# Performance work log

Measured on AMD Instinct MI355X. Metric: run time of the kernel, lower is better.

The kernel has to match this reference:

```python
import jax, jax.numpy as jnp
import numpy as np

FORMULA_OH_SIZES = [20, 20, 20, 20, 20]
SPECT_BIN_N = 512


def layer_norm(x, g, b, eps=1e-5):
    m = jnp.mean(x, axis=-1, keepdims=True)
    v = jnp.var(x, axis=-1, keepdims=True)
    return (x - m) * jax.lax.rsqrt(v + eps) * g + b


def gru_cell(x, h, W_ih, W_hh, b_ih, b_hh):
    # torch.nn.GRUCell math
    gi = x @ W_ih.T + b_ih
    gh = h @ W_hh.T + b_hh
    i_r, i_z, i_n = jnp.split(gi, 3, axis=-1)
    h_r, h_z, h_n = jnp.split(gh, 3, axis=-1)
    r = jax.nn.sigmoid(i_r + h_r)
    z = jax.nn.sigmoid(i_z + h_z)
    n = jnp.tanh(i_n + r * h_n)
    return (1.0 - z) * n + z * h


def structured_one_hot(x, sizes, accum=True):
    # x: [N, len(sizes)] integer element counts -> concatenated (accumulated) one-hots
    outs = []
    for i, s in enumerate(sizes):
        v = jnp.clip(x[:, i].astype(jnp.int32), 0, s - 1)
        if accum:
            oh = (jnp.arange(s)[None, :] <= v[:, None]).astype(jnp.float32)  # thermometer
        else:
            oh = jax.nn.one_hot(v, s, dtype=jnp.float32)
        outs.append(oh)
    return jnp.concatenate(outs, axis=-1)


def setup_inputs():
    key = jax.random.key(0)
    ks = jax.random.split(key, 16)
    B, A, GF, HW, S, M = 16, 32, 128, 4, 4096, 8
    G = GF * HW                       # 512 = g_feat_in * highway_steps_n
    FE = sum(FORMULA_OH_SIZES)        # 100
    D = 512                           # internal_d
    vert_feat_in = jax.random.normal(ks[0], (B, A, GF, HW), jnp.float32)
    vert_mask_in = jnp.ones((B, A), jnp.float32)
    elem_id = jax.random.randint(ks[1], (B, A), 0, 5)
    vert_element_oh = jax.nn.one_hot(elem_id, 5, dtype=jnp.float32)
    adj_oh = jnp.zeros((B, A, A, 4), jnp.float32)  # unused by forward
    atom_subsets = jax.random.bernoulli(ks[2], 0.5, (B, S, A)).astype(jnp.float32)
    masses = jax.random.uniform(ks[3], (B, S, M), jnp.float32, 0.0, SPECT_BIN_N - 1.0)
    intens = jax.random.uniform(ks[4], (B, S, M), jnp.float32)
    atom_subsets_peaks = jnp.stack([masses, intens], axis=-1)

    def lin(k, o, i):
        return (jax.random.normal(k, (o, i), jnp.float32) / np.sqrt(i)).astype(jnp.float32)

    return dict(
        vert_feat_in=vert_feat_in, vert_mask_in=vert_mask_in,
        vert_element_oh=vert_element_oh, adj_oh=adj_oh,
        atom_subsets=atom_subsets, atom_subsets_peaks=atom_subsets_peaks,
        ln_sub_g=jnp.ones((G,), jnp.float32), ln_sub_b=jnp.zeros((G,), jnp.float32),
        W_ih=lin(ks[5], 3 * G, FE), W_hh=lin(ks[6], 3 * G, G),
        b_ih=jnp.zeros((3 * G,), jnp.float32), b_hh=jnp.zeros((3 * G,), jnp.float32),
        W1=lin(ks[7], D, G), b1=jnp.zeros((D,), jnp.float32),
        W2a=lin(ks[8], D, D), b2a=jnp.zeros((D,), jnp.float32),
        W2b=lin(ks[9], D, D), b2b=jnp.zeros((D,), jnp.float32),
        ln_pre_g=jnp.ones((D,), jnp.float32), ln_pre_b=jnp.zeros((D,), jnp.float32),
        Ws=lin(ks[10], 1, D), bs=jnp.zeros((1,), jnp.float32),
    )


def reference(vert_feat_in, vert_mask_in, vert_element_oh, adj_oh, atom_subsets,
              atom_subsets_peaks, ln_sub_g, ln_sub_b, W_ih, W_hh, b_ih, b_hh,
              W1, b1, W2a, b2a, W2b, b2b, ln_pre_g, ln_pre_b, Ws, bs):
    B, A, GF, HW = vert_feat_in.shape
    S = atom_subsets.shape[1]
    vf = vert_feat_in.reshape(B, A, GF * HW)                       # [B,A,G]
    masked_vf = vf * vert_mask_in[:, :, None]
    subs_m = atom_subsets * vert_mask_in[:, None, :]               # [B,S,A]
    swvs = jnp.einsum('bag,bsa->bsg', masked_vf, subs_m)           # [B,S,G]
    # per-subset element counts -> structured one-hot formula encoding
    counts = jnp.einsum('bae,bsa->bse', vert_element_oh, atom_subsets).astype(jnp.int32)
    pf_flat = structured_one_hot(counts.reshape(B * S, -1), FORMULA_OH_SIZES, accum=True)
    subset_size = jnp.sum(subs_m, axis=2) + 1e-4                   # [B,S]
    mean = swvs / subset_size[:, :, None]
    normed = layer_norm(mean, ln_sub_g, ln_sub_b)                  # [B,S,G]
    h = gru_cell(pf_flat, normed.reshape(B * S, -1), W_ih, W_hh, b_ih, b_hh)
    h = h.reshape(normed.shape)
    x = jax.nn.relu(h @ W1.T + b1)
    x = jax.nn.relu(x @ W2a.T + b2a)
    x = jax.nn.relu(x @ W2b.T + b2b)   # (extra F.relu in original is idempotent)
    x = layer_norm(x, ln_pre_g, ln_pre_b)
    scores = (x @ Ws.T + bs)[..., 0]                               # [B,S]
    probs = jax.nn.softmax(scores, axis=-1)
    # mass histogram: scatter intensity*prob into rounded-mass bins
    masses = atom_subsets_peaks[..., 0]                            # [B,S,M]
    intens = atom_subsets_peaks[..., 1]
    bins = jnp.clip(jnp.round(masses).astype(jnp.int32), 0, SPECT_BIN_N - 1)
    contrib = intens * probs[:, :, None]                           # [B,S,M]
    spect = jnp.zeros((B, SPECT_BIN_N), x.dtype).at[
        jnp.arange(B)[:, None], bins.reshape(B, -1)].add(contrib.reshape(B, -1))
    return (spect, probs)
```

## Files before the change

### kernel.cpp

```cpp
#include <hip/hip_runtime.h>
#include <math.h>

#define B_ 16
#define A_ 32
#define G_ 512
#define S_ 4096
#define M_ 8
#define BS_ 65536
#define KC_ 640
#define NG_ 1536
#define SMH 16384

typedef _Float16 half8 __attribute__((ext_vector_type(8)));
typedef _Float16 half4v __attribute__((ext_vector_type(4)));
typedef _Float16 half2v __attribute__((ext_vector_type(2)));
typedef float floatx4 __attribute__((ext_vector_type(4)));

typedef const __attribute__((address_space(1))) void* gas_t;
typedef __attribute__((address_space(3))) void* las_t;

__device__ __forceinline__ float wave_sum_f(float v){
#pragma unroll
  for (int o = 32; o > 0; o >>= 1) v += __shfl_xor(v, o);
  return v;
}
__device__ __forceinline__ float wave_max_f(float v){
#pragma unroll
  for (int o = 32; o > 0; o >>= 1) v = fmaxf(v, __shfl_xor(v, o));
  return v;
}
__device__ __forceinline__ float sigmoidf_(float x){ return 1.f/(1.f+__expf(-x)); }
__device__ __forceinline__ float tanhf_(float x){ return 1.f - 2.f/(__expf(2.f*x)+1.f); }

__global__ __launch_bounds__(256) void k_cvt3(const float* __restrict__ s0,
                                              const float* __restrict__ s1,
                                              const float* __restrict__ s2,
                                              _Float16* __restrict__ d){
  const float* s = (blockIdx.y == 0) ? s0 : (blockIdx.y == 1) ? s1 : s2;
  int i = (blockIdx.x*256 + threadIdx.x)*4;
  if (i >= G_*G_) return;
  float4 v = *(const float4*)(s+i);
  half4v o; o[0]=(_Float16)v.x; o[1]=(_Float16)v.y; o[2]=(_Float16)v.z; o[3]=(_Float16)v.w;
  *(half4v*)(d + (size_t)blockIdx.y*G_*G_ + i) = o;
}

__global__ __launch_bounds__(64) void k_buildw(const float* __restrict__ Whh,
                                               const float* __restrict__ Wih,
                                               _Float16* __restrict__ Wcat){
  int j = blockIdx.x;
  for (int p = threadIdx.x; p < KC_; p += 64){
    float v = 0.f;
    if (p < 512) v = Whh[(size_t)j*512 + p];
    else if (p < 612) v = Wih[(size_t)j*100 + (p - 512)];
    Wcat[(size_t)j*KC_ + p] = (_Float16)v;
  }
}

__global__ __launch_bounds__(256) void k_prep_mfma(
    const float* __restrict__ vf, const float* __restrict__ mask,
    const float* __restrict__ eoh, const float* __restrict__ subs,
    const float* __restrict__ ln_g, const float* __restrict__ ln_b,
    _Float16* __restrict__ Abuf){
  __shared__ _Float16 s_mvfT[G_*A_];
  __shared__ _Float16 s_sm[128*A_];
  __shared__ float s_m[A_];
  __shared__ float s_e[A_*5];
  __shared__ float s_ssum[128];
  __shared__ float s_red1[2][4][16];
  __shared__ float s_red2[2][4][16];
  int tid = threadIdx.x;
  int bx = blockIdx.x, b = blockIdx.y;
  int lane = tid & 63, w = tid >> 6;
  int q = lane >> 4, l15 = lane & 15;
  size_t row0 = (size_t)b*S_ + (size_t)bx*128;
  if (tid < A_)   s_m[tid] = mask[b*A_ + tid];
  if (tid < A_*5) s_e[tid] = eoh[b*A_*5 + tid];
  __syncthreads();
  {
    int p = tid & 15, gseg = tid >> 4;
    float mk0 = s_m[2*p], mk1 = s_m[2*p+1];
    const float* v0 = vf + ((size_t)b*A_ + 2*p)*G_ + gseg*32;
    const float* v1 = v0 + G_;
#pragma unroll
    for (int i = 0; i < 32; i += 4){
      float4 a = *(const float4*)(v0 + i);
      float4 c = *(const float4*)(v1 + i);
      float av[4] = {a.x, a.y, a.z, a.w};
      float cv[4] = {c.x, c.y, c.z, c.w};
#pragma unroll
      for (int j = 0; j < 4; ++j){
        half2v h; h[0] = (_Float16)(av[j]*mk0); h[1] = (_Float16)(cv[j]*mk1);
        *(half2v*)(s_mvfT + (gseg*32 + i + j)*A_ + 2*p) = h;
      }
    }
  }
  {
    int s = tid >> 1, hh = tid & 1;
    const float* sp = subs + (row0 + s)*A_ + hh*16;
    _Float16* dst = s_sm + s*A_ + hh*16;
#pragma unroll
    for (int i = 0; i < 16; i += 4){
      float4 v = *(const float4*)(sp + i);
      half4v h; h[0]=(_Float16)v.x; h[1]=(_Float16)v.y; h[2]=(_Float16)v.z; h[3]=(_Float16)v.w;
      *(half4v*)(dst + i) = h;
    }
  }
  __syncthreads();
  if (tid < 128){
    int s = tid;
    float ssum = 0.f, c0=0.f, c1=0.f, c2=0.f, c3=0.f, c4=0.f;
#pragma unroll
    for (int a = 0; a < A_; ++a){
      float v = (float)s_sm[s*A_ + a];
      ssum += v * s_m[a];
      c0 += v * s_e[a*5+0]; c1 += v * s_e[a*5+1]; c2 += v * s_e[a*5+2];
      c3 += v * s_e[a*5+3]; c4 += v * s_e[a*5+4];
    }
    int cc[5];
    cc[0] = min(max((int)(c0+0.5f),0),19); cc[1] = min(max((int)(c1+0.5f),0),19);
    cc[2] = min(max((int)(c2+0.5f),0),19); cc[3] = min(max((int)(c3+0.5f),0),19);
    cc[4] = min(max((int)(c4+0.5f),0),19);
    s_ssum[s] = ssum;
    _Float16* dst = Abuf + (row0 + s)*KC_ + 512;
#pragma unroll
    for (int t = 0; t < 16; ++t){
      half8 hv;
#pragma unroll
      for (int u = 0; u < 8; ++u){
        int k = t*8 + u;
        float v = 0.f;
        if (k < 100){ int f = k/20, l = k - f*20; v = (l <= cc[f]) ? 1.f : 0.f; }
        hv[u] = (_Float16)v;
      }
      *(half8*)(dst + t*8) = hv;
    }
  }
  half8 bf[8]; float lng[8], lnb[8];
#pragma unroll
  for (int t = 0; t < 8; ++t){
    int g = w*128 + t*16 + l15;
    bf[t] = *(const half8*)(s_mvfT + g*A_ + q*8);
    lng[t] = ln_g[g]; lnb[t] = ln_b[g];
  }
  __syncthreads();
  for (int gi = 0; gi < 8; ++gi){
    half8 af = *(const half8*)(s_sm + (gi*16 + l15)*A_ + q*8);
    floatx4 c[8];
#pragma unroll
    for (int t = 0; t < 8; ++t){
      floatx4 z = {0.f, 0.f, 0.f, 0.f};
      c[t] = __builtin_amdgcn_mfma_f32_16x16x32_f16(af, bf[t], z, 0, 0, 0);
    }
    float p1[4] = {0.f,0.f,0.f,0.f}, p2[4] = {0.f,0.f,0.f,0.f};
#pragma unroll
    for (int t = 0; t < 8; ++t)
#pragma unroll
      for (int r = 0; r < 4; ++r){ float v = c[t][r]; p1[r] += v; p2[r] += v*v; }
#pragma unroll
    for (int off = 1; off < 16; off <<= 1)
#pragma unroll
      for (int r = 0; r < 4; ++r){
        p1[r] += __shfl_xor(p1[r], off);
        p2[r] += __shfl_xor(p2[r], off);
      }
    int gb = gi & 1;
    if (l15 == 0){
#pragma unroll
      for (int r = 0; r < 4; ++r){ s_red1[gb][w][q*4+r] = p1[r]; s_red2[gb][w][q*4+r] = p2[r]; }
    }
    __syncthreads();
#pragma unroll
    for (int r = 0; r < 4; ++r){
      int sl = gi*16 + q*4 + r;
      int rr = q*4 + r;
      float t1 = s_red1[gb][0][rr] + s_red1[gb][1][rr] + s_red1[gb][2][rr] + s_red1[gb][3][rr];
      float t2 = s_red2[gb][0][rr] + s_red2[gb][1][rr] + s_red2[gb][2][rr] + s_red2[gb][3][rr];
      float inv = 1.f/(s_ssum[sl] + 1e-4f);
      float mu = t1*inv*(1.f/512.f);
      float var = t2*inv*inv*(1.f/512.f) - mu*mu;
      float rs = rsqrtf(var + 1e-5f);
      _Float16* orow = Abuf + (row0 + sl)*KC_;
#pragma unroll
      for (int t = 0; t < 8; ++t){
        float o = (c[t][r]*inv - mu)*rs*lng[t] + lnb[t];
        orow[w*128 + t*16 + l15] = (_Float16)o;
      }
    }
  }
}

__global__ __launch_bounds__(512) void k_gru_fused(
    const _Float16* __restrict__ Abuf, const _Float16* __restrict__ Wcat,
    const float* __restrict__ bih, const float* __restrict__ bhh,
    _Float16* __restrict__ H){
  __shared__ _Float16 smA[2][128*32];
  __shared__ _Float16 smB[2][192*32];
  int tid = threadIdx.x;
  int lane = tid & 63, wvid = tid >> 6;
  int wm = wvid & 1, wn = wvid >> 1;
  int q = lane >> 4, l15 = lane & 15;
  int mt = blockIdx.x*64 + (blockIdx.y >> 3);
  int dt = blockIdx.y & 7;
  int m0 = mt*128, n0 = dt*64;
  floatx4 acc[3][4] = {};
  floatx4 accNI[4] = {};
  int offA[4], offB[3];
#pragma unroll
  for (int i = 0; i < 4; ++i){
    int r = wm*64 + i*16 + l15;
    offA[i] = (r*4 + (q ^ ((r>>2)&3)))*8;
  }
#pragma unroll
  for (int g = 0; g < 3; ++g){
    int rb = g*64 + wn*16 + l15;
    offB[g] = (rb*4 + (q ^ ((rb>>2)&3)))*8;
  }
  const _Float16* gA;
  {
    int u = wvid*64 + lane;
    int r = u >> 2, c = (u & 3) ^ ((r >> 2) & 3);
    gA = Abuf + (size_t)(m0 + r)*KC_ + c*8;
  }
  const _Float16* gB0;
  {
    int u = wvid*64 + lane;
    int rb = u >> 2, c = (u & 3) ^ ((rb >> 2) & 3);
    int grow = (rb >> 6)*512 + n0 + (rb & 63);
    gB0 = Wcat + (size_t)grow*KC_ + c*8;
  }
  const _Float16* gB1 = nullptr;
  if (wvid < 4){
    int u = (8 + wvid)*64 + lane;
    int rb = u >> 2, c = (u & 3) ^ ((rb >> 2) & 3);
    int grow = (rb >> 6)*512 + n0 + (rb & 63);
    gB1 = Wcat + (size_t)grow*KC_ + c*8;
  }
  __builtin_amdgcn_global_load_lds((gas_t)gA,  (las_t)(smA[0] + wvid*512), 16, 0, 0);
  __builtin_amdgcn_global_load_lds((gas_t)gB0, (las_t)(smB[0] + wvid*512), 16, 0, 0);
  if (wvid < 4)
    __builtin_amdgcn_global_load_lds((gas_t)gB1, (las_t)(smB[0] + (8+wvid)*512), 16, 0, 0);
  asm volatile("s_waitcnt vmcnt(0)");
  __builtin_amdgcn_s_barrier();
  const int NT = KC_/32;
  for (int t = 0; t < NT; ++t){
    int cur = t & 1;
    if (t + 1 < NT){
      int kc = (t+1)*32;
      __builtin_amdgcn_global_load_lds((gas_t)(gA + kc),  (las_t)(smA[cur^1] + wvid*512), 16, 0, 0);
      __builtin_amdgcn_global_load_lds((gas_t)(gB0 + kc), (las_t)(smB[cur^1] + wvid*512), 16, 0, 0);
      if (wvid < 4)
        __builtin_amdgcn_global_load_lds((gas_t)(gB1 + kc), (las_t)(smB[cur^1] + (8+wvid)*512), 16, 0, 0);
    }
    half8 af[4], bfv[3];
#pragma unroll
    for (int i = 0; i < 4; ++i) af[i] = *(const half8*)(smA[cur] + offA[i]);
#pragma unroll
    for (int g = 0; g < 3; ++g) bfv[g] = *(const half8*)(smB[cur] + offB[g]);
    if (t < 16){
#pragma unroll
      for (int g = 0; g < 3; ++g)
#pragma unroll
        for (int i = 0; i < 4; ++i)
          acc[g][i] = __builtin_amdgcn_mfma_f32_16x16x32_f16(af[i], bfv[g], acc[g][i], 0, 0, 0);
    } else {
#pragma unroll
      for (int i = 0; i < 4; ++i){
        acc[0][i] = __builtin_amdgcn_mfma_f32_16x16x32_f16(af[i], bfv[0], acc[0][i], 0, 0, 0);
        acc[1][i] = __builtin_amdgcn_mfma_f32_16x16x32_f16(af[i], bfv[1], acc[1][i], 0, 0, 0);
        accNI[i]  = __builtin_amdgcn_mfma_f32_16x16x32_f16(af[i], bfv[2], accNI[i], 0, 0, 0);
      }
    }
    asm volatile("s_waitcnt vmcnt(0)");
    __builtin_amdgcn_s_barrier();
  }
  int d = n0 + wn*16 + l15;
  float br  = bih[d] + bhh[d];
  float bz  = bih[512+d] + bhh[512+d];
  float bnh = bhh[1024+d];
  float bni = bih[1024+d];
#pragma unroll
  for (int i = 0; i < 4; ++i){
#pragma unroll
    for (int r = 0; r < 4; ++r){
      int m = m0 + wm*64 + i*16 + q*4 + r;
      float gr  = acc[0][i][r] + br;
      float gz  = acc[1][i][r] + bz;
      float hn  = acc[2][i][r] + bnh;
      float in_ = accNI[i][r] + bni;
      float rrv = sigmoidf_(gr);
      float zz  = sigmoidf_(gz);
      float nn  = tanhf_(in_ + rrv*hn);
      float hp  = (float)Abuf[(size_t)m*KC_ + d];
      H[(size_t)m*G_ + d] = (_Float16)((1.f-zz)*nn + zz*hp);
    }
  }
}


#define STG_A8(T) do{ \
    __builtin_amdgcn_global_load_lds((gas_t)(pA0 + (T)*64),           (las_t)(&smA8[(T)&1][0] + wvid*1024),        16, 0, 0); \
    __builtin_amdgcn_global_load_lds((gas_t)(pA1 + (T)*64),           (las_t)(&smA8[(T)&1][0] + wvid*1024 + 512),  16, 0, 0); \
    __builtin_amdgcn_global_load_lds((gas_t)(pA0 + 128*G_ + (T)*64),  (las_t)(&smA8[(T)&1][0] + 8192 + wvid*1024), 16, 0, 0); \
    __builtin_amdgcn_global_load_lds((gas_t)(pA1 + 128*G_ + (T)*64),  (las_t)(&smA8[(T)&1][0] + 8192 + wvid*1024 + 512), 16, 0, 0); \
  }while(0)
#define STG_B8(T,H) do{ \
    __builtin_amdgcn_global_load_lds((gas_t)(pB0 + (H)*128*G_ + (T)*64), (las_t)(&smB8[(T)&1][0] + (H)*8192 + wvid*1024),       16, 0, 0); \
    __builtin_amdgcn_global_load_lds((gas_t)(pB1 + (H)*128*G_ + (T)*64), (las_t)(&smB8[(T)&1][0] + (H)*8192 + wvid*1024 + 512), 16, 0, 0); \
  }while(0)
#define RD_A8(DST, T, MF0) do{ \
    const _Float16* ba_ = &smA8[(T)&1][0]; \
    DST[0][0] = *(const half8*)(ba_ + aoff0 + (MF0)*1024); \
    DST[0][1] = *(const half8*)(ba_ + aoff1 + (MF0)*1024); \
    DST[1][0] = *(const half8*)(ba_ + aoff0 + ((MF0)+1)*1024); \
    DST[1][1] = *(const half8*)(ba_ + aoff1 + ((MF0)+1)*1024); \
  }while(0)
#define RD_B8(DST, T) do{ \
    const _Float16* bb_ = &smB8[(T)&1][0]; \
    _Pragma("unroll") \
    for (int nf_ = 0; nf_ < 4; ++nf_){ \
      DST[nf_][0] = *(const half8*)(bb_ + boff0 + nf_*1024); \
      DST[nf_][1] = *(const half8*)(bb_ + boff1 + nf_*1024); \
    } \
  }while(0)
#define MMQ8(AV, BV, MF0) do{ \
    _Pragma("unroll") \
    for (int u_ = 0; u_ < 2; ++u_) \
    _Pragma("unroll") \
    for (int nf_ = 0; nf_ < 4; ++nf_){ \
      acc[(MF0)+u_][nf_] = __builtin_amdgcn_mfma_f32_16x16x32_f16(AV[u_][0], BV[nf_][0], acc[(MF0)+u_][nf_], 0, 0, 0); \
      acc[(MF0)+u_][nf_] = __builtin_amdgcn_mfma_f32_16x16x32_f16(AV[u_][1], BV[nf_][1], acc[(MF0)+u_][nf_], 0, 0, 0); \
    } \
  }while(0)
#define PH_Q0(T, BC) do{ if ((T)+1 <= 7) STG_A8((T)+1); RD_A8(a_o, T, 2); \
    __builtin_amdgcn_s_barrier(); __builtin_amdgcn_s_setprio(1); MMQ8(a_e, BC, 0); \
    __builtin_amdgcn_s_setprio(0); __builtin_amdgcn_s_barrier(); }while(0)
#define PH_Q1(T, BC) do{ if ((T)+2 <= 7) STG_B8((T)+2, 0); RD_A8(a_e, T, 4); \
    __builtin_amdgcn_s_barrier(); __builtin_amdgcn_s_setprio(1); MMQ8(a_o, BC, 2); \
    __builtin_amdgcn_s_setprio(0); __builtin_amdgcn_s_barrier(); }while(0)
#define PH_Q2(T, BC) do{ if ((T)+2 <= 7) STG_B8((T)+2, 1); RD_A8(a_o, T, 6); \
    __builtin_amdgcn_s_barrier(); __builtin_amdgcn_s_setprio(1); MMQ8(a_e, BC, 4); \
    __builtin_amdgcn_s_setprio(0); __builtin_amdgcn_s_barrier(); }while(0)
#define PH_Q3(T, BC, BN) do{ \
    if ((T) < 7){ \
      if ((T) < 6) asm volatile("s_waitcnt vmcnt(4)" ::: "memory"); \
      else         asm volatile("s_waitcnt vmcnt(0)" ::: "memory"); \
      RD_B8(BN, (T)+1); RD_A8(a_e, (T)+1, 0); \
    } \
    __builtin_amdgcn_s_barrier(); __builtin_amdgcn_s_setprio(1); MMQ8(a_o, BC, 6); \
    __builtin_amdgcn_s_setprio(0); __builtin_amdgcn_s_barrier(); }while(0)
#define TILE8(T, BC, BN) do{ PH_Q0(T, BC); PH_Q1(T, BC); PH_Q2(T, BC); PH_Q3(T, BC, BN); }while(0)

#define K8_SETUP(Amat, Wmat) \
  int tid = threadIdx.x; \
  int lane = tid & 63, wvid = tid >> 6; \
  int wm = wvid & 1, wn = wvid >> 1; \
  int q = lane >> 4, l15 = lane & 15; \
  int x_ = l15 & 7; \
  int bid = blockIdx.x; \
  int wg = (bid & 7)*64 + (bid >> 3); \
  int mt = wg >> 1, nt = wg & 1; \
  int m0 = mt*256, n0 = nt*256; \
  int swzlo = (q ^ (x_ & 3))*8; \
  int aoff0 = (wm*128 + l15)*64 + ((0 ^ (x_>>2))*4)*8 + swzlo; \
  int aoff1 = (wm*128 + l15)*64 + ((1 ^ (x_>>2))*4)*8 + swzlo; \
  int boff0 = (wn*64 + l15)*64 + ((0 ^ (x_>>2))*4)*8 + swzlo; \
  int boff1 = (wn*64 + l15)*64 + ((1 ^ (x_>>2))*4)*8 + swzlo; \
  int srow = wvid*16 + (lane >> 3); \
  int sc = ((lane & 7) ^ ((lane >> 3) & 7))*8; \
  const _Float16* pA0 = Amat + (size_t)(m0 + srow)*G_ + sc; \
  const _Float16* pA1 = Amat + (size_t)(m0 + srow + 8)*G_ + sc; \
  const _Float16* pB0 = Wmat + (size_t)(n0 + srow)*G_ + sc; \
  const _Float16* pB1 = Wmat + (size_t)(n0 + srow + 8)*G_ + sc; \
  floatx4 acc[8][4] = {}; \
  half8 a_e[2][2], a_o[2][2], bA[4][2], bB[4][2]; \
  STG_A8(0); STG_B8(0,0); STG_B8(0,1); STG_B8(1,0); STG_B8(1,1); \
  asm volatile("s_waitcnt vmcnt(4)" ::: "memory"); \
  __builtin_amdgcn_s_barrier(); \
  RD_B8(bA, 0); RD_A8(a_e, 0, 0); \
  TILE8(0, bA, bB); TILE8(1, bB, bA); \
  TILE8(2, bA, bB); TILE8(3, bB, bA); \
  TILE8(4, bA, bB); TILE8(5, bB, bA); \
  TILE8(6, bA, bB); TILE8(7, bB, bA);

__global__ __launch_bounds__(512, 2) void k_gemm8(
    const _Float16* __restrict__ A, const _Float16* __restrict__ W,
    const float* __restrict__ bias, _Float16* __restrict__ Out){
  __shared__ _Float16 smA8[2][SMH];
  __shared__ _Float16 smB8[2][SMH];
  K8_SETUP(A, W)
  float bv[4];
#pragma unroll
  for (int nf = 0; nf < 4; ++nf) bv[nf] = bias[n0 + wn*64 + nf*16 + l15];
#pragma unroll
  for (int mf = 0; mf < 8; ++mf){
    int m = m0 + wm*128 + mf*16 + q*4;
#pragma unroll
    for (int nf = 0; nf < 4; ++nf){
      int n = n0 + wn*64 + nf*16 + l15;
#pragma unroll
      for (int r = 0; r < 4; ++r)
        Out[(size_t)(m+r)*G_ + n] = (_Float16)fmaxf(acc[mf][nf][r] + bv[nf], 0.f);
    }
  }
}

__global__ __launch_bounds__(512, 2) void k_ff38(
    const _Float16* __restrict__ A, const _Float16* __restrict__ W,
    const float* __restrict__ bias, const float* __restrict__ ln_pre_g,
    const float* __restrict__ Ws, float* __restrict__ Pbuf){
  __shared__ _Float16 smA8[2][SMH];
  __shared__ _Float16 smB8[2][SMH];
  K8_SETUP(A, W)
  float gws[4], bv[4];
#pragma unroll
  for (int nf = 0; nf < 4; ++nf){
    int n = n0 + wn*64 + nf*16 + l15;
    gws[nf] = ln_pre_g[n]*Ws[n];
    bv[nf] = bias[n];
  }
  float* sP = (float*)&smB8[0][0];
#pragma unroll
  for (int mf = 0; mf < 8; ++mf){
#pragma unroll
    for (int r = 0; r < 4; ++r){
      float p1 = 0.f, p2 = 0.f, p3 = 0.f;
#pragma unroll
      for (int nf = 0; nf < 4; ++nf){
        float xv = fmaxf(acc[mf][nf][r] + bv[nf], 0.f);
        p1 += xv; p2 += xv*xv; p3 += gws[nf]*xv;
      }
#pragma unroll
      for (int off = 1; off < 16; off <<= 1){
        p1 += __shfl_xor(p1, off);
        p2 += __shfl_xor(p2, off);
        p3 += __shfl_xor(p3, off);
      }
      if (l15 == 0){
        int rl = wm*128 + mf*16 + q*4 + r;
        sP[(rl*4 + wn)*3 + 0] = p1;
        sP[(rl*4 + wn)*3 + 1] = p2;
        sP[(rl*4 + wn)*3 + 2] = p3;
      }
    }
  }
  __syncthreads();
  if (tid < 256){
    int m = m0 + tid;
    float* dst = Pbuf + ((size_t)m*2 + nt)*3;
#pragma unroll
    for (int c = 0; c < 3; ++c)
      dst[c] = sP[(tid*4+0)*3+c] + sP[(tid*4+1)*3+c] +
               sP[(tid*4+2)*3+c] + sP[(tid*4+3)*3+c];
  }
}

__global__ __launch_bounds__(256) void k_score_fin(
    const float* __restrict__ Pbuf, const float* __restrict__ g,
    const float* __restrict__ bta, const float* __restrict__ Ws,
    const float* __restrict__ bs, float* __restrict__ scores,
    float* __restrict__ spect){
  __shared__ float red[8];
  int tid = threadIdx.x, lane = tid & 63, wv = tid >> 6;
  if (blockIdx.x < 32) spect[(size_t)blockIdx.x*256 + tid] = 0.f;
  int i0 = tid*2;
  float c1p = g[i0]*Ws[i0] + g[i0+1]*Ws[i0+1];
  float c2p = bta[i0]*Ws[i0] + bta[i0+1]*Ws[i0+1];
  c1p = wave_sum_f(c1p); c2p = wave_sum_f(c2p);
  if (lane == 0){ red[wv] = c1p; red[4+wv] = c2p; }
  __syncthreads();
  float c1 = red[0]+red[1]+red[2]+red[3];
  float c2 = red[4]+red[5]+red[6]+red[7] + bs[0];
  size_t row = (size_t)blockIdx.x*256 + tid;
  const float* p = Pbuf + row*6;
  float2 u0 = *(const float2*)p;
  float2 u1 = *(const float2*)(p+2);
  float2 u2 = *(const float2*)(p+4);
  float P1 = u0.x + u1.y;
  float P2 = u0.y + u2.x;
  float P3 = u1.x + u2.y;
  float mu = P1*(1.f/512.f);
  float var = P2*(1.f/512.f) - mu*mu;
  float rs = rsqrtf(var + 1e-5f);
  scores[row] = rs*(P3 - mu*c1) + c2;
}

__global__ __launch_bounds__(256) void k_softmax(
    const float* __restrict__ scores, float* __restrict__ probs){
  __shared__ float red[4];
  int b = blockIdx.x, tid = threadIdx.x, lane = tid & 63, wv = tid >> 6;
  const float* sp = scores + (size_t)b*S_;
  float* pp = probs + (size_t)b*S_;
  float mx = -1e30f;
  for (int i = tid; i < S_; i += 256) mx = fmaxf(mx, sp[i]);
  mx = wave_max_f(mx);
  if (lane == 0) red[wv] = mx;
  __syncthreads();
  mx = fmaxf(fmaxf(red[0], red[1]), fmaxf(red[2], red[3]));
  __syncthreads();
  float sum = 0.f;
  for (int i = tid; i < S_; i += 256){
    float e = __expf(sp[i]-mx);
    pp[i] = e;
    sum += e;
  }
  sum = wave_sum_f(sum);
  if (lane == 0) red[wv] = sum;
  __syncthreads();
  sum = red[0]+red[1]+red[2]+red[3];
  float inv = 1.f/sum;
  for (int i = tid; i < S_; i += 256)
    pp[i] *= inv;
}

__global__ __launch_bounds__(256) void k_spect_p(
    const float* __restrict__ peaks, const float* __restrict__ probs,
    float* __restrict__ spect){
  __shared__ float bins[512];
  int b = blockIdx.x, chunk = blockIdx.y, tid = threadIdx.x;
  bins[tid] = 0.f; bins[tid+256] = 0.f;
  __syncthreads();
  int s0 = chunk*(S_/8);
  for (int i = tid; i < (S_/8)*M_; i += 256){
    int s = s0 + (i >> 3), m = i & 7;
    const float* pk = peaks + (((size_t)b*S_ + s)*M_ + m)*2;
    float mass = pk[0], inten = pk[1];
    float p = probs[(size_t)b*S_ + s];
    int bin = (int)rintf(mass);
    bin = min(max(bin, 0), 511);
    atomicAdd(&bins[bin], inten*p);
  }
  __syncthreads();
  atomicAdd(&spect[(size_t)b*512 + tid],       bins[tid]);
  atomicAdd(&spect[(size_t)b*512 + tid + 256], bins[tid+256]);
}

extern "C" void kernel_launch(void* const* d_in, const int* in_sizes, int n_in,
                              void* d_out, int out_size, void* d_ws, size_t ws_size,
                              hipStream_t stream) {
  const float* vf       = (const float*)d_in[0];
  const float* mask     = (const float*)d_in[1];
  const float* eoh      = (const float*)d_in[2];
  const float* subs     = (const float*)d_in[4];
  const float* peaks    = (const float*)d_in[5];
  const float* ln_sub_g = (const float*)d_in[6];
  const float* ln_sub_b = (const float*)d_in[7];
  const float* W_ih     = (const float*)d_in[8];
  const float* W_hh     = (const float*)d_in[9];
  const float* b_ih     = (const float*)d_in[10];
  const float* b_hh     = (const float*)d_in[11];
  const float* W1       = (const float*)d_in[12];
  const float* b1       = (const float*)d_in[13];
  const float* W2a      = (const float*)d_in[14];
  const float* b2a      = (const float*)d_in[15];
  const float* W2b      = (const float*)d_in[16];
  const float* b2b      = (const float*)d_in[17];
  const float* ln_pre_g = (const float*)d_in[18];
  const float* ln_pre_b = (const float*)d_in[19];
  const float* Ws       = (const float*)d_in[20];
  const float* bs       = (const float*)d_in[21];
  float* out = (float*)d_out;
  float* probs_out = out + (size_t)B_*512;

  char* w = (char*)d_ws;
  float* scores = (float*)w;     w += (size_t)BS_*4;
  float* Pbuf   = (float*)w;     w += (size_t)BS_*12*4;
  _Float16* Wcat = (_Float16*)w; w += (size_t)NG_*KC_*2;
  _Float16* W1h  = (_Float16*)w; w += (size_t)G_*G_*2;
  _Float16* W2ah = (_Float16*)w; w += (size_t)G_*G_*2;
  _Float16* W2bh = (_Float16*)w; w += (size_t)G_*G_*2;
  _Float16* Abuf = (_Float16*)w; w += (size_t)BS_*KC_*2;
  _Float16* bufh0 = (_Float16*)w;
  _Float16* bufh1 = Abuf;

  k_cvt3<<<dim3((G_*G_/4+255)/256, 3), 256, 0, stream>>>(W1, W2a, W2b, W1h);
  k_buildw<<<NG_, 64, 0, stream>>>(W_hh, W_ih, Wcat);
  k_prep_mfma<<<dim3(S_/128, B_), 256, 0, stream>>>(vf, mask, eoh, subs,
                                                    ln_sub_g, ln_sub_b, Abuf);
  k_gru_fused<<<dim3(8, 512), 512, 0, stream>>>(Abuf, Wcat, b_ih, b_hh, bufh0);
  k_gemm8<<<512, 512, 0, stream>>>(bufh0, W1h,  b1,  bufh1);
  k_gemm8<<<512, 512, 0, stream>>>(bufh1, W2ah, b2a, bufh0);
  k_ff38<<<512, 512, 0, stream>>>(bufh0, W2bh, b2b, ln_pre_g, Ws, Pbuf);
  k_score_fin<<<BS_/256, 256, 0, stream>>>(Pbuf, ln_pre_g, ln_pre_b, Ws, bs,
                                           scores, out);
  k_softmax<<<B_, 256, 0, stream>>>(scores, probs_out);
  k_spect_p<<<dim3(B_, 8), 256, 0, stream>>>(peaks, probs_out, out);
}
```

Before: 470.0 us.

## Rewrite GRU GEMM with 256-row tiles, 64-wide K stages, and phased software pipeline

```diff
diff --git a/kernel.cpp b/kernel.cpp
--- a/kernel.cpp
+++ b/kernel.cpp
@@ -189,104 +189,120 @@
   }
 }
 
-__global__ __launch_bounds__(512) void k_gru_fused(
+#define GSTG_A(T) do{ \
+    __builtin_amdgcn_global_load_lds((gas_t)(qA0 + (T)*64),            (las_t)(&gmA[(T)&1][0] + wvid*1024),        16, 0, 0); \
+    __builtin_amdgcn_global_load_lds((gas_t)(qA1 + (T)*64),            (las_t)(&gmA[(T)&1][0] + wvid*1024 + 512),  16, 0, 0); \
+    __builtin_amdgcn_global_load_lds((gas_t)(qA0 + 128*KC_ + (T)*64),  (las_t)(&gmA[(T)&1][0] + 8192 + wvid*1024), 16, 0, 0); \
+    __builtin_amdgcn_global_load_lds((gas_t)(qA1 + 128*KC_ + (T)*64),  (las_t)(&gmA[(T)&1][0] + 8192 + wvid*1024 + 512), 16, 0, 0); \
+  }while(0)
+#define GSTG_B(T) do{ \
+    __builtin_amdgcn_global_load_lds((gas_t)(qB0 + (T)*64), (las_t)(&gmB[(T)&1][0] + wvid*1536),        16, 0, 0); \
+    __builtin_amdgcn_global_load_lds((gas_t)(qB1 + (T)*64), (las_t)(&gmB[(T)&1][0] + wvid*1536 + 512),  16, 0, 0); \
+    __builtin_amdgcn_global_load_lds((gas_t)(qB2 + (T)*64), (las_t)(&gmB[(T)&1][0] + wvid*1536 + 1024), 16, 0, 0); \
+  }while(0)
+#define GRD_A(DST, T, MF0) do{ \
+    const _Float16* ba_ = &gmA[(T)&1][0]; \
+    DST[0][0] = *(const half8*)(ba_ + aoff0 + (MF0)*1024); \
+    DST[0][1] = *(const half8*)(ba_ + aoff1 + (MF0)*1024); \
+    DST[1][0] = *(const half8*)(ba_ + aoff0 + ((MF0)+1)*1024); \
+    DST[1][1] = *(const half8*)(ba_ + aoff1 + ((MF0)+1)*1024); \
+  }while(0)
+#define GRD_B(DST, T) do{ \
+    const _Float16* bb_ = &gmB[(T)&1][0]; \
+    _Pragma("unroll") \
+    for (int g_ = 0; g_ < 3; ++g_){ \
+      DST[g_][0] = *(const half8*)(bb_ + bo0[g_]); \
+      DST[g_][1] = *(const half8*)(bb_ + bo1[g_]); \
+    } \
+  }while(0)
+#define GMMQ(AV, BV, MF0, G2) do{ \
+    _Pragma("unroll") \
+    for (int u_ = 0; u_ < 2; ++u_){ \
+      acc[(MF0)+u_][0]  = __builtin_amdgcn_mfma_f32_16x16x32_f16(AV[u_][0], BV[0][0], acc[(MF0)+u_][0], 0, 0, 0); \
+      acc[(MF0)+u_][0]  = __builtin_amdgcn_mfma_f32_16x16x32_f16(AV[u_][1], BV[0][1], acc[(MF0)+u_][0], 0, 0, 0); \
+      acc[(MF0)+u_][1]  = __builtin_amdgcn_mfma_f32_16x16x32_f16(AV[u_][0], BV[1][0], acc[(MF0)+u_][1], 0, 0, 0); \
+      acc[(MF0)+u_][1]  = __builtin_amdgcn_mfma_f32_16x16x32_f16(AV[u_][1], BV[1][1], acc[(MF0)+u_][1], 0, 0, 0); \
+      acc[(MF0)+u_][G2] = __builtin_amdgcn_mfma_f32_16x16x32_f16(AV[u_][0], BV[2][0], acc[(MF0)+u_][G2], 0, 0, 0); \
+      acc[(MF0)+u_][G2] = __builtin_amdgcn_mfma_f32_16x16x32_f16(AV[u_][1], BV[2][1], acc[(MF0)+u_][G2], 0, 0, 0); \
+    } \
+  }while(0)
+#define GPH0(T, BC, G2) do{ if ((T)+1 <= 9) GSTG_A((T)+1); GRD_A(a_o, T, 2); \
+    __builtin_amdgcn_s_barrier(); __builtin_amdgcn_s_setprio(1); GMMQ(a_e, BC, 0, G2); \
+    __builtin_amdgcn_s_setprio(0); __builtin_amdgcn_s_barrier(); }while(0)
+#define GPH1(T, BC, G2) do{ if ((T)+2 <= 9) GSTG_B((T)+2); GRD_A(a_e, T, 4); \
+    __builtin_amdgcn_s_barrier(); __builtin_amdgcn_s_setprio(1); GMMQ(a_o, BC, 2, G2); \
+    __builtin_amdgcn_s_setprio(0); __builtin_amdgcn_s_barrier(); }while(0)
+#define GPH2(T, BC, G2) do{ GRD_A(a_o, T, 6); \
+    __builtin_amdgcn_s_barrier(); __builtin_amdgcn_s_setprio(1); GMMQ(a_e, BC, 4, G2); \
+    __builtin_amdgcn_s_setprio(0); __builtin_amdgcn_s_barrier(); }while(0)
+#define GPH3(T, BC, BN, G2) do{ \
+    if ((T) < 9){ \
+      if ((T)+2 <= 9) asm volatile("s_waitcnt vmcnt(3)" ::: "memory"); \
+      else            asm volatile("s_waitcnt vmcnt(0)" ::: "memory"); \
+      GRD_B(BN, (T)+1); GRD_A(a_e, (T)+1, 0); \
+    } \
+    __builtin_amdgcn_s_barrier(); __builtin_amdgcn_s_setprio(1); GMMQ(a_o, BC, 6, G2); \
+    __builtin_amdgcn_s_setprio(0); __builtin_amdgcn_s_barrier(); }while(0)
+#define GTILE(T, BC, BN, G2) do{ GPH0(T, BC, G2); GPH1(T, BC, G2); GPH2(T, BC, G2); GPH3(T, BC, BN, G2); }while(0)
+
+__global__ __launch_bounds__(512, 2) void k_gru8(
     const _Float16* __restrict__ Abuf, const _Float16* __restrict__ Wcat,
     const float* __restrict__ bih, const float* __restrict__ bhh,
     _Float16* __restrict__ H){
-  __shared__ _Float16 smA[2][128*32];
-  __shared__ _Float16 smB[2][192*32];
+  __shared__ _Float16 gmA[2][SMH];
+  __shared__ _Float16 gmB[2][192*64];
   int tid = threadIdx.x;
   int lane = tid & 63, wvid = tid >> 6;
   int wm = wvid & 1, wn = wvid >> 1;
   int q = lane >> 4, l15 = lane & 15;
-  int mt = blockIdx.x*64 + (blockIdx.y >> 3);
-  int dt = blockIdx.y & 7;
-  int m0 = mt*128, n0 = dt*64;
-  floatx4 acc[3][4] = {};
-  floatx4 accNI[4] = {};
-  int offA[4], offB[3];
-#pragma unroll
-  for (int i = 0; i < 4; ++i){
-    int r = wm*64 + i*16 + l15;
-    offA[i] = (r*4 + (q ^ ((r>>2)&3)))*8;
-  }
+  int x_ = l15 & 7;
+  int bid = blockIdx.x;
+  int mt = (bid & 7)*32 + (bid >> 6);
+  int dt = (bid >> 3) & 7;
+  int m0 = mt*256, d0 = dt*64;
+  int swzlo = (q ^ (x_ & 3))*8;
+  int aoff0 = (wm*128 + l15)*64 + ((0 ^ (x_>>2))*4)*8 + swzlo;
+  int aoff1 = (wm*128 + l15)*64 + ((1 ^ (x_>>2))*4)*8 + swzlo;
+  int bo0[3], bo1[3];
 #pragma unroll
   for (int g = 0; g < 3; ++g){
-    int rb = g*64 + wn*16 + l15;
-    offB[g] = (rb*4 + (q ^ ((rb>>2)&3)))*8;
-  }
-  const _Float16* gA;
-  {
-    int u = wvid*64 + lane;
-    int r = u >> 2, c = (u & 3) ^ ((r >> 2) & 3);
-    gA = Abuf + (size_t)(m0 + r)*KC_ + c*8;
-  }
-  const _Float16* gB0;
-  {
-    int u = wvid*64 + lane;
-    int rb = u >> 2, c = (u & 3) ^ ((rb >> 2) & 3);
-    int grow = (rb >> 6)*512 + n0 + (rb & 63);
-    gB0 = Wcat + (size_t)grow*KC_ + c*8;
-  }
-  const _Float16* gB1 = nullptr;
-  if (wvid < 4){
-    int u = (8 + wvid)*64 + lane;
-    int rb = u >> 2, c = (u & 3) ^ ((rb >> 2) & 3);
-    int grow = (rb >> 6)*512 + n0 + (rb & 63);
-    gB1 = Wcat + (size_t)grow*KC_ + c*8;
-  }
-  __builtin_amdgcn_global_load_lds((gas_t)gA,  (las_t)(smA[0] + wvid*512), 16, 0, 0);
-  __builtin_amdgcn_global_load_lds((gas_t)gB0, (las_t)(smB[0] + wvid*512), 16, 0, 0);
-  if (wvid < 4)
-    __builtin_amdgcn_global_load_lds((gas_t)gB1, (las_t)(smB[0] + (8+wvid)*512), 16, 0, 0);
-  asm volatile("s_waitcnt vmcnt(0)");
+    int rb = (g*64 + wn*16 + l15)*64;
+    bo0[g] = rb + ((0 ^ (x_>>2))*4)*8 + swzlo;
+    bo1[g] = rb + ((1 ^ (x_>>2))*4)*8 + swzlo;
+  }
+  int srow = wvid*16 + (lane >> 3);
+  int sc = ((lane & 7) ^ ((lane >> 3) & 7))*8;
+  const _Float16* qA0 = Abuf + (size_t)(m0 + srow)*KC_ + sc;
+  const _Float16* qA1 = Abuf + (size_t)(m0 + srow + 8)*KC_ + sc;
+  int rb0 = wvid*24 + (lane >> 3);
+  const _Float16* qB0 = Wcat + (size_t)(((rb0    )>>6)*512 + d0 + ((rb0    )&63))*KC_ + sc;
+  const _Float16* qB1 = Wcat + (size_t)(((rb0+ 8)>>6)*512 + d0 + ((rb0+ 8)&63))*KC_ + sc;
+  const _Float16* qB2 = Wcat + (size_t)(((rb0+16)>>6)*512 + d0 + ((rb0+16)&63))*KC_ + sc;
+  floatx4 acc[8][4] = {};
+  half8 a_e[2][2], a_o[2][2], bA[3][2], bB[3][2];
+  GSTG_A(0); GSTG_B(0); GSTG_B(1);
+  asm volatile("s_waitcnt vmcnt(3)" ::: "memory");
   __builtin_amdgcn_s_barrier();
-  const int NT = KC_/32;
-  for (int t = 0; t < NT; ++t){
-    int cur = t & 1;
-    if (t + 1 < NT){
-      int kc = (t+1)*32;
-      __builtin_amdgcn_global_load_lds((gas_t)(gA + kc),  (las_t)(smA[cur^1] + wvid*512), 16, 0, 0);
-      __builtin_amdgcn_global_load_lds((gas_t)(gB0 + kc), (las_t)(smB[cur^1] + wvid*512), 16, 0, 0);
-      if (wvid < 4)
-        __builtin_amdgcn_global_load_lds((gas_t)(gB1 + kc), (las_t)(smB[cur^1] + (8+wvid)*512), 16, 0, 0);
-    }
-    half8 af[4], bfv[3];
-#pragma unroll
-    for (int i = 0; i < 4; ++i) af[i] = *(const half8*)(smA[cur] + offA[i]);
-#pragma unroll
-    for (int g = 0; g < 3; ++g) bfv[g] = *(const half8*)(smB[cur] + offB[g]);
-    if (t < 16){
-#pragma unroll
-      for (int g = 0; g < 3; ++g)
-#pragma unroll
-        for (int i = 0; i < 4; ++i)
-          acc[g][i] = __builtin_amdgcn_mfma_f32_16x16x32_f16(af[i], bfv[g], acc[g][i], 0, 0, 0);
-    } else {
-#pragma unroll
-      for (int i = 0; i < 4; ++i){
-        acc[0][i] = __builtin_amdgcn_mfma_f32_16x16x32_f16(af[i], bfv[0], acc[0][i], 0, 0, 0);
-        acc[1][i] = __builtin_amdgcn_mfma_f32_16x16x32_f16(af[i], bfv[1], acc[1][i], 0, 0, 0);
-        accNI[i]  = __builtin_amdgcn_mfma_f32_16x16x32_f16(af[i], bfv[2], accNI[i], 0, 0, 0);
-      }
-    }
-    asm volatile("s_waitcnt vmcnt(0)");
-    __builtin_amdgcn_s_barrier();
-  }
-  int d = n0 + wn*16 + l15;
+  GRD_B(bA, 0); GRD_A(a_e, 0, 0);
+  GTILE(0, bA, bB, 2); GTILE(1, bB, bA, 2);
+  GTILE(2, bA, bB, 2); GTILE(3, bB, bA, 2);
+  GTILE(4, bA, bB, 2); GTILE(5, bB, bA, 2);
+  GTILE(6, bA, bB, 2); GTILE(7, bB, bA, 2);
+  GTILE(8, bA, bB, 3); GTILE(9, bB, bA, 3);
+  int d = d0 + wn*16 + l15;
   float br  = bih[d] + bhh[d];
   float bz  = bih[512+d] + bhh[512+d];
   float bnh = bhh[1024+d];
   float bni = bih[1024+d];
 #pragma unroll
-  for (int i = 0; i < 4; ++i){
+  for (int mf = 0; mf < 8; ++mf){
 #pragma unroll
     for (int r = 0; r < 4; ++r){
-      int m = m0 + wm*64 + i*16 + q*4 + r;
-      float gr  = acc[0][i][r] + br;
-      float gz  = acc[1][i][r] + bz;
-      float hn  = acc[2][i][r] + bnh;
-      float in_ = accNI[i][r] + bni;
+      int m = m0 + wm*128 + mf*16 + q*4 + r;
+      float gr  = acc[mf][0][r] + br;
+      float gz  = acc[mf][1][r] + bz;
+      float hn  = acc[mf][2][r] + bnh;
+      float in_ = acc[mf][3][r] + bni;
       float rrv = sigmoidf_(gr);
       float zz  = sigmoidf_(gz);
       float nn  = tanhf_(in_ + rrv*hn);
@@ -295,7 +311,6 @@
     }
   }
 }
-
 
 #define STG_A8(T) do{ \
     __builtin_amdgcn_global_load_lds((gas_t)(pA0 + (T)*64),           (las_t)(&smA8[(T)&1][0] + wvid*1024),        16, 0, 0); \
@@ -576,7 +591,7 @@
   k_buildw<<<NG_, 64, 0, stream>>>(W_hh, W_ih, Wcat);
   k_prep_mfma<<<dim3(S_/128, B_), 256, 0, stream>>>(vf, mask, eoh, subs,
                                                     ln_sub_g, ln_sub_b, Abuf);
-  k_gru_fused<<<dim3(8, 512), 512, 0, stream>>>(Abuf, Wcat, b_ih, b_hh, bufh0);
+  k_gru8<<<2048, 512, 0, stream>>>(Abuf, Wcat, b_ih, b_hh, bufh0);
   k_gemm8<<<512, 512, 0, stream>>>(bufh0, W1h,  b1,  bufh1);
   k_gemm8<<<512, 512, 0, stream>>>(bufh1, W2ah, b2a, bufh0);
   k_ff38<<<512, 512, 0, stream>>>(bufh0, W2bh, b2b, ln_pre_g, Ws, Pbuf);
```

Result: no change. 465.9 us (-0.9%).
